# Kernel optimization log

Hardware: AMD Instinct MI355X
Metric: run time of the kernel (lower is better)

## Reference

```python
import jax, jax.numpy as jnp
import numpy as np

HEADS = 4
OUT = 64  # hidden_channels


def gat_conv(x, src, dst, N, W, att_src, att_dst, bias):
    # x: [N, Fin] -> h: [N, H, C]
    h = (x @ W).reshape(N, HEADS, OUT)
    a_s = (h * att_src).sum(-1)  # [N, H]
    a_d = (h * att_dst).sum(-1)  # [N, H]
    logits = jax.nn.leaky_relu(a_s[src] + a_d[dst], negative_slope=0.2)  # [E, H]
    # segment softmax over incoming edges of each destination node
    m = jax.ops.segment_max(logits, dst, num_segments=N)
    e = jnp.exp(logits - m[dst])
    z = jax.ops.segment_sum(e, dst, num_segments=N)
    alpha = e / (z[dst] + 1e-16)
    out = jax.ops.segment_sum(h[src] * alpha[:, :, None], dst, num_segments=N)
    return out.reshape(N, HEADS * OUT) + bias


def setup_inputs() -> dict:
    key = jax.random.key(0)
    ks = jax.random.split(key, 16)
    N, E, F = 50000, 800000, 128
    HC = HEADS * OUT  # 256
    s = 0.1
    return {
        "x": jax.random.normal(ks[0], (N, F), jnp.float32),
        "edge_index": jax.random.randint(ks[1], (2, E), 0, N, dtype=jnp.int32),
        "W1": jax.random.normal(ks[2], (F, HC), jnp.float32) * s,
        "as1": jax.random.normal(ks[3], (1, HEADS, OUT), jnp.float32) * s,
        "ad1": jax.random.normal(ks[4], (1, HEADS, OUT), jnp.float32) * s,
        "b1": jnp.zeros((HC,), jnp.float32),
        "W2": jax.random.normal(ks[5], (HC, HC), jnp.float32) * s,
        "as2": jax.random.normal(ks[6], (1, HEADS, OUT), jnp.float32) * s,
        "ad2": jax.random.normal(ks[7], (1, HEADS, OUT), jnp.float32) * s,
        "b2": jnp.zeros((HC,), jnp.float32),
        "lw1": jax.random.normal(ks[8], (HC, OUT), jnp.float32) * s,
        "lb1": jnp.zeros((OUT,), jnp.float32),
        "lw2": jax.random.normal(ks[9], (OUT, 2), jnp.float32) * s,
        "lb2": jnp.zeros((2,), jnp.float32),
    }


def reference(x, edge_index, W1, as1, ad1, b1, W2, as2, ad2, b2, lw1, lb1, lw2, lb2):
    N = x.shape[0]
    # PyG GATConv default add_self_loops=True
    loop = jnp.arange(N, dtype=edge_index.dtype)
    src = jnp.concatenate([edge_index[0], loop])
    dst = jnp.concatenate([edge_index[1], loop])
    h = jax.nn.elu(gat_conv(x, src, dst, N, W1, as1, ad1, b1))
    # dropout is identity at inference
    h = jax.nn.elu(gat_conv(h, src, dst, N, W2, as2, ad2, b2))
    h = jax.nn.relu(h @ lw1 + lb1)
    return jax.nn.log_softmax(h @ lw2 + lb2, axis=1)
```

## Files before the change

kernel.cpp:

```cpp
#include <hip/hip_runtime.h>
#include <math.h>


typedef __attribute__((ext_vector_type(8))) _Float16 half8v;
typedef __attribute__((ext_vector_type(4))) float f32x4;

__device__ __forceinline__ float lrelu(float x) { return x > 0.f ? x : 0.2f * x; }
__device__ __forceinline__ float elu1(float x) { return x > 0.f ? x : (__expf(x) - 1.f); }

__global__ void convert_weights_kernel(const float* __restrict__ W1, const float* __restrict__ W2,
                                       const float* __restrict__ lw1,
                                       _Float16* __restrict__ o1, _Float16* __restrict__ o2,
                                       _Float16* __restrict__ o3, int* __restrict__ indeg,
                                       int N) {
  int t = blockIdx.x * blockDim.x + threadIdx.x;
  if (t < 32768) {
    int n = t >> 7, k = t & 127;
    o1[t] = (_Float16)W1[(long)k * 256 + n];
  } else if (t < 98304) {
    int i = t - 32768;
    int n = i >> 8, k = i & 255;
    o2[i] = (_Float16)W2[(long)k * 256 + n];
  } else if (t < 114688) {
    int i = t - 98304;
    int n = i >> 8, k = i & 255;
    o3[i] = (_Float16)lw1[(long)k * 64 + n];
  } else if (t < 114688 + N) {
    indeg[t - 114688] = 0;
  }
}

__global__ void count_kernel(const int* __restrict__ dst, int E, int* __restrict__ indeg) {
  int e = blockIdx.x * blockDim.x + threadIdx.x;
  if (e < E) atomicAdd(&indeg[dst[e]], 1);
}

__global__ void scan_block_kernel(const int* __restrict__ in, int* __restrict__ incl,
                                  int* __restrict__ bsum, int N) {
  __shared__ int wsum[16];
  int gid = blockIdx.x * 1024 + threadIdx.x;
  int lane = threadIdx.x & 63, w = threadIdx.x >> 6;
  int v = (gid < N) ? in[gid] : 0;
  int sv = v;
#pragma unroll
  for (int o = 1; o < 64; o <<= 1) {
    int t = __shfl_up(sv, o);
    if (lane >= o) sv += t;
  }
  if (lane == 63) wsum[w] = sv;
  __syncthreads();
  if (w == 0) {
    int bs = (lane < 16) ? wsum[lane] : 0;
#pragma unroll
    for (int o = 1; o < 16; o <<= 1) {
      int t = __shfl_up(bs, o);
      if (lane >= o) bs += t;
    }
    if (lane < 16) wsum[lane] = bs;
  }
  __syncthreads();
  if (w > 0) sv += wsum[w - 1];
  if (gid < N) incl[gid] = sv;
  if (threadIdx.x == 1023) bsum[blockIdx.x] = sv;
}

__global__ void scan_finalize_kernel(const int* __restrict__ in, const int* __restrict__ incl,
                                     const int* __restrict__ bsum, int* __restrict__ off,
                                     int* __restrict__ cursor, int N) {
  int gid = blockIdx.x * blockDim.x + threadIdx.x;
  if (gid >= N) return;
  int b = gid >> 10;
  int carry = 0;
  for (int k = 0; k < b; ++k) carry += bsum[k];
  int ic = incl[gid] + carry;
  off[gid + 1] = ic;
  cursor[gid] = ic - in[gid];
  if (gid == 0) off[0] = 0;
}

__global__ void fill_kernel(const int* __restrict__ src, const int* __restrict__ dst, int E,
                            int* __restrict__ cursor, int* __restrict__ csr_src) {
  int e = blockIdx.x * blockDim.x + threadIdx.x;
  if (e < E) {
    int pos = atomicAdd(&cursor[dst[e]], 1);
    csr_src[pos] = src[e];
  }
}

template <typename AT>
__launch_bounds__(256)
__global__ void mfma_gemm_attn_kernel(const AT* __restrict__ A,
                                      const _Float16* __restrict__ B,
                                      const float* __restrict__ att_s,
                                      const float* __restrict__ att_d,
                                      _Float16* __restrict__ C,
                                      float* __restrict__ a_s, float* __restrict__ a_d,
                                      int M, int K) {
  __shared__ _Float16 As[128][40];
  __shared__ _Float16 Bs[128][40];
  int tid = threadIdx.x;
  int bm = blockIdx.y * 128, bn = blockIdx.x * 128;
  int lane = tid & 63, wave = tid >> 6;
  int srow = tid >> 2, sch = (tid & 3) * 8;
  const AT* Ap0 = A + (long)(bm + srow) * K + sch;
  const AT* Ap1 = A + (long)(bm + 64 + srow) * K + sch;
  const _Float16* Bp0 = B + (long)(bn + srow) * K + sch;
  const _Float16* Bp1 = B + (long)(bn + 64 + srow) * K + sch;
  bool aok0 = (bm + srow) < M, aok1 = (bm + 64 + srow) < M;
  int fm = lane & 15, fq = lane >> 4;
  int wr = wave >> 1, wc = wave & 1;
  f32x4 acc[4][4];
#pragma unroll
  for (int mi = 0; mi < 4; ++mi)
#pragma unroll
    for (int ni = 0; ni < 4; ++ni) acc[mi][ni] = (f32x4){0.f, 0.f, 0.f, 0.f};
  for (int k0 = 0; k0 < K; k0 += 32) {
    half8v a80 = {0, 0, 0, 0, 0, 0, 0, 0}, a81 = {0, 0, 0, 0, 0, 0, 0, 0};
    if constexpr (sizeof(AT) == 4) {
      if (aok0) {
        float4 f0 = *(const float4*)(Ap0 + k0);
        float4 f1 = *(const float4*)(Ap0 + k0 + 4);
        a80 = (half8v){(_Float16)f0.x, (_Float16)f0.y, (_Float16)f0.z, (_Float16)f0.w,
                       (_Float16)f1.x, (_Float16)f1.y, (_Float16)f1.z, (_Float16)f1.w};
      }
      if (aok1) {
        float4 f0 = *(const float4*)(Ap1 + k0);
        float4 f1 = *(const float4*)(Ap1 + k0 + 4);
        a81 = (half8v){(_Float16)f0.x, (_Float16)f0.y, (_Float16)f0.z, (_Float16)f0.w,
                       (_Float16)f1.x, (_Float16)f1.y, (_Float16)f1.z, (_Float16)f1.w};
      }
    } else {
      if (aok0) a80 = *(const half8v*)(Ap0 + k0);
      if (aok1) a81 = *(const half8v*)(Ap1 + k0);
    }
    uint4 vb0 = *(const uint4*)(Bp0 + k0);
    uint4 vb1 = *(const uint4*)(Bp1 + k0);
    *(half8v*)&As[srow][sch] = a80;
    *(half8v*)&As[64 + srow][sch] = a81;
    *(uint4*)&Bs[srow][sch] = vb0;
    *(uint4*)&Bs[64 + srow][sch] = vb1;
    __syncthreads();
    half8v ah[4], bh[4];
#pragma unroll
    for (int i = 0; i < 4; ++i) ah[i] = *(const half8v*)&As[wr * 64 + i * 16 + fm][fq * 8];
#pragma unroll
    for (int i = 0; i < 4; ++i) bh[i] = *(const half8v*)&Bs[wc * 64 + i * 16 + fm][fq * 8];
#pragma unroll
    for (int mi = 0; mi < 4; ++mi)
#pragma unroll
      for (int ni = 0; ni < 4; ++ni)
        acc[mi][ni] = __builtin_amdgcn_mfma_f32_16x16x32_f16(ah[mi], bh[ni], acc[mi][ni], 0, 0, 0);
    __syncthreads();
  }
  int headi = blockIdx.x * 2 + wc;
  int cbase = bn + wc * 64;
  float asv[4], adv[4];
#pragma unroll
  for (int ni = 0; ni < 4; ++ni) {
    int col = cbase + ni * 16 + fm;
    asv[ni] = att_s[col];
    adv[ni] = att_d[col];
  }
#pragma unroll
  for (int mi = 0; mi < 4; ++mi) {
    int rowb = bm + wr * 64 + mi * 16 + fq * 4;
#pragma unroll
    for (int r = 0; r < 4; ++r) {
      int row = rowb + r;
      float sp = 0.f, dp = 0.f;
#pragma unroll
      for (int ni = 0; ni < 4; ++ni) {
        float v = acc[mi][ni][r];
        sp = fmaf(v, asv[ni], sp);
        dp = fmaf(v, adv[ni], dp);
        if (row < M) C[(long)row * 256 + cbase + ni * 16 + fm] = (_Float16)v;
      }
#pragma unroll
      for (int o = 1; o < 16; o <<= 1) {
        sp += __shfl_xor(sp, o);
        dp += __shfl_xor(dp, o);
      }
      if (fm == 0 && row < M) {
        a_s[(long)row * 4 + headi] = sp;
        a_d[(long)row * 4 + headi] = dp;
      }
    }
  }
}

__launch_bounds__(256)
__global__ void head_mfma_kernel(const _Float16* __restrict__ A, const _Float16* __restrict__ B,
                                 const float* __restrict__ lb1, const float* __restrict__ lw2,
                                 const float* __restrict__ lb2, float* __restrict__ out, int M) {
  __shared__ _Float16 As[128][40];
  __shared__ _Float16 Bs[64][40];
  int tid = threadIdx.x;
  int bm = blockIdx.x * 128;
  int lane = tid & 63, wave = tid >> 6;
  int srow = tid >> 2, sch = (tid & 3) * 8;
  const _Float16* Ap0 = A + (long)(bm + srow) * 256 + sch;
  const _Float16* Ap1 = A + (long)(bm + 64 + srow) * 256 + sch;
  const _Float16* Bp = B + (long)srow * 256 + sch;
  bool aok0 = (bm + srow) < M, aok1 = (bm + 64 + srow) < M;
  int fm = lane & 15, fq = lane >> 4;
  f32x4 acc[2][4];
#pragma unroll
  for (int mi = 0; mi < 2; ++mi)
#pragma unroll
    for (int ni = 0; ni < 4; ++ni) acc[mi][ni] = (f32x4){0.f, 0.f, 0.f, 0.f};
  for (int k0 = 0; k0 < 256; k0 += 32) {
    half8v a80 = {0, 0, 0, 0, 0, 0, 0, 0}, a81 = {0, 0, 0, 0, 0, 0, 0, 0};
    if (aok0) a80 = *(const half8v*)(Ap0 + k0);
    if (aok1) a81 = *(const half8v*)(Ap1 + k0);
    uint4 vb = *(const uint4*)(Bp + k0);
    *(half8v*)&As[srow][sch] = a80;
    *(half8v*)&As[64 + srow][sch] = a81;
    *(uint4*)&Bs[srow][sch] = vb;
    __syncthreads();
    half8v ah[2], bh[4];
#pragma unroll
    for (int mi = 0; mi < 2; ++mi)
      ah[mi] = *(const half8v*)&As[wave * 32 + mi * 16 + fm][fq * 8];
#pragma unroll
    for (int ni = 0; ni < 4; ++ni) bh[ni] = *(const half8v*)&Bs[ni * 16 + fm][fq * 8];
#pragma unroll
    for (int mi = 0; mi < 2; ++mi)
#pragma unroll
      for (int ni = 0; ni < 4; ++ni)
        acc[mi][ni] = __builtin_amdgcn_mfma_f32_16x16x32_f16(ah[mi], bh[ni], acc[mi][ni], 0, 0, 0);
    __syncthreads();
  }
  float lb1c[4], w20[4], w21[4];
#pragma unroll
  for (int ni = 0; ni < 4; ++ni) {
    int col = ni * 16 + fm;
    lb1c[ni] = lb1[col];
    w20[ni] = lw2[col * 2 + 0];
    w21[ni] = lw2[col * 2 + 1];
  }
  float b20 = lb2[0], b21 = lb2[1];
#pragma unroll
  for (int mi = 0; mi < 2; ++mi) {
#pragma unroll
    for (int r = 0; r < 4; ++r) {
      float v0 = 0.f, v1 = 0.f;
#pragma unroll
      for (int ni = 0; ni < 4; ++ni) {
        float s = fmaxf(acc[mi][ni][r] + lb1c[ni], 0.f);
        v0 = fmaf(s, w20[ni], v0);
        v1 = fmaf(s, w21[ni], v1);
      }
#pragma unroll
      for (int o = 1; o < 16; o <<= 1) {
        v0 += __shfl_xor(v0, o);
        v1 += __shfl_xor(v1, o);
      }
      if (fm == 0) {
        int row = bm + wave * 32 + mi * 16 + fq * 4 + r;
        if (row < M) {
          v0 += b20;
          v1 += b21;
          float mx = fmaxf(v0, v1);
          float ls = mx + logf(expf(v0 - mx) + expf(v1 - mx));
          out[(long)row * 2 + 0] = v0 - ls;
          out[(long)row * 2 + 1] = v1 - ls;
        }
      }
    }
  }
}

__launch_bounds__(256)
__global__ void gat_aggregate_exp_kernel(const _Float16* __restrict__ h,
                                         const float* __restrict__ a_s,
                                         const float* __restrict__ a_d,
                                         const int* __restrict__ off,
                                         const int* __restrict__ csr_src,
                                         const float* __restrict__ bias,
                                         _Float16* __restrict__ outp, int N) {
  int wid = (blockIdx.x * blockDim.x + threadIdx.x) >> 6;
  int lane = threadIdx.x & 63;
  if (wid >= N) return;
  int c = lane & 31, hlf = lane >> 5, head4 = c >> 3;
  int h1 = lane & 3, sl1 = lane >> 2;
  int beg = off[wid], cnt = off[wid + 1] - beg;
  float ad_h1 = a_d[wid * 4 + h1];
  float psl = __expf(lrelu(a_s[wid * 4 + h1] + ad_h1));
  float pself = __shfl(psl, head4);
  float z = 0.f;
  float acc[8] = {};
  if (hlf == 0) {
    z = pself;
    half8v sr = *(const half8v*)(h + (long)wid * 256 + c * 8);
#pragma unroll
    for (int i = 0; i < 8; ++i) acc[i] = pself * (float)sr[i];
  }
  for (int c0 = 0; c0 < cnt; c0 += 16) {
    int i2 = c0 + (lane & 15);
    int sv = (i2 < cnt) ? csr_src[beg + i2] : 0;
    int i1 = c0 + sl1;
    int spi = __shfl(sv, sl1);
    float pv = (i1 < cnt) ? __expf(lrelu(a_s[(long)spi * 4 + h1] + ad_h1)) : 0.f;
#pragma unroll 4
    for (int j = 0; j < 16; j += 2) {
      if (c0 + j >= cnt) break;
      int e = j + hlf;
      int s = __shfl(sv, e);
      float p = __shfl(pv, e * 4 + head4);
      z += p;
      half8v rv = *(const half8v*)(h + (long)s * 256 + c * 8);
      acc[0] = fmaf(p, (float)rv[0], acc[0]);
      acc[1] = fmaf(p, (float)rv[1], acc[1]);
      acc[2] = fmaf(p, (float)rv[2], acc[2]);
      acc[3] = fmaf(p, (float)rv[3], acc[3]);
      acc[4] = fmaf(p, (float)rv[4], acc[4]);
      acc[5] = fmaf(p, (float)rv[5], acc[5]);
      acc[6] = fmaf(p, (float)rv[6], acc[6]);
      acc[7] = fmaf(p, (float)rv[7], acc[7]);
    }
  }
  z += __shfl_xor(z, 32);
#pragma unroll
  for (int i = 0; i < 8; ++i) acc[i] += __shfl_xor(acc[i], 32);
  if (hlf == 0) {
    float inv = 1.f / z;
    half8v o;
#pragma unroll
    for (int i = 0; i < 8; ++i) o[i] = (_Float16)elu1(fmaf(acc[i], inv, bias[c * 8 + i]));
    *(half8v*)(outp + (long)wid * 256 + c * 8) = o;
  }
}

static inline int cdiv(int a, int b) { return (a + b - 1) / b; }

extern "C" void kernel_launch(void* const* d_in, const int* in_sizes, int n_in,
                              void* d_out, int out_size, void* d_ws, size_t ws_size,
                              hipStream_t stream) {
  const float* x = (const float*)d_in[0];
  const int* ei = (const int*)d_in[1];
  const float* W1 = (const float*)d_in[2];
  const float* as1 = (const float*)d_in[3];
  const float* ad1 = (const float*)d_in[4];
  const float* b1 = (const float*)d_in[5];
  const float* W2 = (const float*)d_in[6];
  const float* as2 = (const float*)d_in[7];
  const float* ad2 = (const float*)d_in[8];
  const float* b2 = (const float*)d_in[9];
  const float* lw1 = (const float*)d_in[10];
  const float* lb1 = (const float*)d_in[11];
  const float* lw2 = (const float*)d_in[12];
  const float* lb2 = (const float*)d_in[13];
  float* out = (float*)d_out;

  int N = in_sizes[0] / 128;
  int E = in_sizes[1] / 2;
  int Mp = cdiv(N, 128) * 128;

  char* ws = (char*)d_ws;
  _Float16* Wt1 = (_Float16*)ws; ws += 256 * 128 * 2;
  _Float16* Wt2 = (_Float16*)ws; ws += 256 * 256 * 2;
  _Float16* WL = (_Float16*)ws; ws += 64 * 256 * 2;
  _Float16* C = (_Float16*)ws; ws += (size_t)Mp * 256 * 2;
  _Float16* h2 = (_Float16*)ws; ws += (size_t)Mp * 256 * 2;
  float* aS = (float*)ws; ws += (size_t)N * 4 * 4;
  float* aD = (float*)ws; ws += (size_t)N * 4 * 4;
  int* csr_src = (int*)ws; ws += (size_t)E * 4;
  int* indeg = (int*)ws; ws += (size_t)N * 4;
  int* cursor = (int*)ws; ws += (size_t)N * 4;
  int* off = (int*)ws; ws += (size_t)(N + 4) * 4;
  int* incl = (int*)ws; ws += (size_t)N * 4;
  int* bsum = (int*)ws; ws += 64 * 4;

  const int* e_src = ei;
  const int* e_dst = ei + E;
  int nb = cdiv(N, 1024);

  convert_weights_kernel<<<cdiv(114688 + N, 256), 256, 0, stream>>>(W1, W2, lw1, Wt1, Wt2, WL,
                                                                    indeg, N);

  count_kernel<<<cdiv(E, 256), 256, 0, stream>>>(e_dst, E, indeg);
  scan_block_kernel<<<nb, 1024, 0, stream>>>(indeg, incl, bsum, N);
  scan_finalize_kernel<<<cdiv(N, 256), 256, 0, stream>>>(indeg, incl, bsum, off, cursor, N);
  fill_kernel<<<cdiv(E, 256), 256, 0, stream>>>(e_src, e_dst, E, cursor, csr_src);

  mfma_gemm_attn_kernel<float><<<dim3(2, Mp / 128), 256, 0, stream>>>(x, Wt1, as1, ad1, C, aS, aD,
                                                                      N, 128);
  gat_aggregate_exp_kernel<<<cdiv(N, 4), 256, 0, stream>>>(C, aS, aD, off, csr_src, b1, h2, N);

  mfma_gemm_attn_kernel<_Float16><<<dim3(2, Mp / 128), 256, 0, stream>>>(h2, Wt2, as2, ad2, C, aS,
                                                                         aD, N, 256);
  gat_aggregate_exp_kernel<<<cdiv(N, 4), 256, 0, stream>>>(C, aS, aD, off, csr_src, b2, h2, N);

  head_mfma_kernel<<<Mp / 128, 256, 0, stream>>>(h2, WL, lb1, lw2, lb2, out, N);
}
```

Baseline: 380.1 us.

## Preload whole B panel into LDS and stream A fragments directly from global

The GEMM+attention and head kernels now load the full K-depth slice of the weight panel (64 columns) into shared memory once. Each wave then reads its A fragments straight from global memory into MFMA registers, with no per-k-step A staging and no barriers inside the k loop. The GEMM grid changes from 128x128 tiles to 128-row x 64-column tiles (one head per block). This removes per-iteration syncthreads and LDS traffic for A. In exchange, A rows are reread by four column-panel blocks, and the uncoalesced per-lane row loads may cost more memory traffic.

```diff
diff --git a/kernel.cpp b/kernel.cpp
--- a/kernel.cpp
+++ b/kernel.cpp
@@ -87,73 +87,71 @@
   }
 }
 
-template <typename AT>
+template <typename AT, int K>
 __launch_bounds__(256)
-__global__ void mfma_gemm_attn_kernel(const AT* __restrict__ A,
-                                      const _Float16* __restrict__ B,
-                                      const float* __restrict__ att_s,
-                                      const float* __restrict__ att_d,
-                                      _Float16* __restrict__ C,
-                                      float* __restrict__ a_s, float* __restrict__ a_d,
-                                      int M, int K) {
-  __shared__ _Float16 As[128][40];
-  __shared__ _Float16 Bs[128][40];
+__global__ void gemm_stream_attn_kernel(const AT* __restrict__ A,
+                                        const _Float16* __restrict__ B,
+                                        const float* __restrict__ att_s,
+                                        const float* __restrict__ att_d,
+                                        _Float16* __restrict__ C,
+                                        float* __restrict__ a_s, float* __restrict__ a_d,
+                                        int M) {
+  constexpr int NK = K / 32;
+  __shared__ _Float16 Bs[NK][64][40];
   int tid = threadIdx.x;
-  int bm = blockIdx.y * 128, bn = blockIdx.x * 128;
   int lane = tid & 63, wave = tid >> 6;
-  int srow = tid >> 2, sch = (tid & 3) * 8;
-  const AT* Ap0 = A + (long)(bm + srow) * K + sch;
-  const AT* Ap1 = A + (long)(bm + 64 + srow) * K + sch;
-  const _Float16* Bp0 = B + (long)(bn + srow) * K + sch;
-  const _Float16* Bp1 = B + (long)(bn + 64 + srow) * K + sch;
-  bool aok0 = (bm + srow) < M, aok1 = (bm + 64 + srow) < M;
+  int bm = blockIdx.y * 128;
+  int panel = blockIdx.x;
+  int cbase = panel * 64;
+  {
+    int col = tid >> 2, kc = (tid & 3) * 8;
+    const _Float16* Bp = B + (long)(cbase + col) * K + kc;
+#pragma unroll
+    for (int ks = 0; ks < NK; ++ks)
+      *(uint4*)&Bs[ks][col][kc] = *(const uint4*)(Bp + ks * 32);
+  }
+  __syncthreads();
   int fm = lane & 15, fq = lane >> 4;
-  int wr = wave >> 1, wc = wave & 1;
-  f32x4 acc[4][4];
-#pragma unroll
-  for (int mi = 0; mi < 4; ++mi)
+  int row0 = bm + wave * 32 + fm;
+  int row1 = row0 + 16;
+  const AT* Ap0 = A + (long)row0 * K + fq * 8;
+  const AT* Ap1 = A + (long)row1 * K + fq * 8;
+  bool ok0 = row0 < M, ok1 = row1 < M;
+  f32x4 acc[2][4];
+#pragma unroll
+  for (int mi = 0; mi < 2; ++mi)
 #pragma unroll
     for (int ni = 0; ni < 4; ++ni) acc[mi][ni] = (f32x4){0.f, 0.f, 0.f, 0.f};
-  for (int k0 = 0; k0 < K; k0 += 32) {
-    half8v a80 = {0, 0, 0, 0, 0, 0, 0, 0}, a81 = {0, 0, 0, 0, 0, 0, 0, 0};
+#pragma unroll
+  for (int ks = 0; ks < NK; ++ks) {
+    half8v a0 = {0, 0, 0, 0, 0, 0, 0, 0}, a1 = {0, 0, 0, 0, 0, 0, 0, 0};
     if constexpr (sizeof(AT) == 4) {
-      if (aok0) {
-        float4 f0 = *(const float4*)(Ap0 + k0);
-        float4 f1 = *(const float4*)(Ap0 + k0 + 4);
-        a80 = (half8v){(_Float16)f0.x, (_Float16)f0.y, (_Float16)f0.z, (_Float16)f0.w,
-                       (_Float16)f1.x, (_Float16)f1.y, (_Float16)f1.z, (_Float16)f1.w};
-      }
-      if (aok1) {
-        float4 f0 = *(const float4*)(Ap1 + k0);
-        float4 f1 = *(const float4*)(Ap1 + k0 + 4);
-        a81 = (half8v){(_Float16)f0.x, (_Float16)f0.y, (_Float16)f0.z, (_Float16)f0.w,
-                       (_Float16)f1.x, (_Float16)f1.y, (_Float16)f1.z, (_Float16)f1.w};
+      if (ok0) {
+        float4 f0 = *(const float4*)(Ap0 + ks * 32);
+        float4 f1 = *(const float4*)(Ap0 + ks * 32 + 4);
+        a0 = (half8v){(_Float16)f0.x, (_Float16)f0.y, (_Float16)f0.z, (_Float16)f0.w,
+                      (_Float16)f1.x, (_Float16)f1.y, (_Float16)f1.z, (_Float16)f1.w};
+      }
+      if (ok1) {
+        float4 f0 = *(const float4*)(Ap1 + ks * 32);
+        float4 f1 = *(const float4*)(Ap1 + ks * 32 + 4);
+        a1 = (half8v){(_Float16)f0.x, (_Float16)f0.y, (_Float16)f0.z, (_Float16)f0.w,
+                      (_Float16)f1.x, (_Float16)f1.y, (_Float16)f1.z, (_Float16)f1.w};
       }
     } else {
-      if (aok0) a80 = *(const half8v*)(Ap0 + k0);
-      if (aok1) a81 = *(const half8v*)(Ap1 + k0);
-    }
-    uint4 vb0 = *(const uint4*)(Bp0 + k0);
-    uint4 vb1 = *(const uint4*)(Bp1 + k0);
-    *(half8v*)&As[srow][sch] = a80;
-    *(half8v*)&As[64 + srow][sch] = a81;
-    *(uint4*)&Bs[srow][sch] = vb0;
-    *(uint4*)&Bs[64 + srow][sch] = vb1;
-    __syncthreads();
-    half8v ah[4], bh[4];
-#pragma unroll
-    for (int i = 0; i < 4; ++i) ah[i] = *(const half8v*)&As[wr * 64 + i * 16 + fm][fq * 8];
-#pragma unroll
-    for (int i = 0; i < 4; ++i) bh[i] = *(const half8v*)&Bs[wc * 64 + i * 16 + fm][fq * 8];
-#pragma unroll
-    for (int mi = 0; mi < 4; ++mi)
-#pragma unroll
-      for (int ni = 0; ni < 4; ++ni)
-        acc[mi][ni] = __builtin_amdgcn_mfma_f32_16x16x32_f16(ah[mi], bh[ni], acc[mi][ni], 0, 0, 0);
-    __syncthreads();
-  }
-  int headi = blockIdx.x * 2 + wc;
-  int cbase = bn + wc * 64;
+      if (ok0) a0 = *(const half8v*)(Ap0 + ks * 32);
+      if (ok1) a1 = *(const half8v*)(Ap1 + ks * 32);
+    }
+    half8v bh[4];
+#pragma unroll
+    for (int ni = 0; ni < 4; ++ni) bh[ni] = *(const half8v*)&Bs[ks][ni * 16 + fm][fq * 8];
+#pragma unroll
+    for (int ni = 0; ni < 4; ++ni) {
+      acc[0][ni] = __builtin_amdgcn_mfma_f32_16x16x32_f16(a0, bh[ni], acc[0][ni], 0, 0, 0);
+      acc[1][ni] = __builtin_amdgcn_mfma_f32_16x16x32_f16(a1, bh[ni], acc[1][ni], 0, 0, 0);
+    }
+  }
+  int headi = panel;
   float asv[4], adv[4];
 #pragma unroll
   for (int ni = 0; ni < 4; ++ni) {
@@ -162,8 +160,8 @@
     adv[ni] = att_d[col];
   }
 #pragma unroll
-  for (int mi = 0; mi < 4; ++mi) {
-    int rowb = bm + wr * 64 + mi * 16 + fq * 4;
+  for (int mi = 0; mi < 2; ++mi) {
+    int rowb = bm + wave * 32 + mi * 16 + fq * 4;
 #pragma unroll
     for (int r = 0; r < 4; ++r) {
       int row = rowb + r;
@@ -189,46 +187,46 @@
 }
 
 __launch_bounds__(256)
-__global__ void head_mfma_kernel(const _Float16* __restrict__ A, const _Float16* __restrict__ B,
-                                 const float* __restrict__ lb1, const float* __restrict__ lw2,
-                                 const float* __restrict__ lb2, float* __restrict__ out, int M) {
-  __shared__ _Float16 As[128][40];
-  __shared__ _Float16 Bs[64][40];
+__global__ void head_stream_kernel(const _Float16* __restrict__ A, const _Float16* __restrict__ B,
+                                   const float* __restrict__ lb1, const float* __restrict__ lw2,
+                                   const float* __restrict__ lb2, float* __restrict__ out, int M) {
+  constexpr int NK = 8;
+  __shared__ _Float16 Bs[NK][64][40];
   int tid = threadIdx.x;
+  int lane = tid & 63, wave = tid >> 6;
   int bm = blockIdx.x * 128;
-  int lane = tid & 63, wave = tid >> 6;
-  int srow = tid >> 2, sch = (tid & 3) * 8;
-  const _Float16* Ap0 = A + (long)(bm + srow) * 256 + sch;
-  const _Float16* Ap1 = A + (long)(bm + 64 + srow) * 256 + sch;
-  const _Float16* Bp = B + (long)srow * 256 + sch;
-  bool aok0 = (bm + srow) < M, aok1 = (bm + 64 + srow) < M;
+  {
+    int col = tid >> 2, kc = (tid & 3) * 8;
+    const _Float16* Bp = B + (long)col * 256 + kc;
+#pragma unroll
+    for (int ks = 0; ks < NK; ++ks)
+      *(uint4*)&Bs[ks][col][kc] = *(const uint4*)(Bp + ks * 32);
+  }
+  __syncthreads();
   int fm = lane & 15, fq = lane >> 4;
+  int row0 = bm + wave * 32 + fm;
+  int row1 = row0 + 16;
+  const _Float16* Ap0 = A + (long)row0 * 256 + fq * 8;
+  const _Float16* Ap1 = A + (long)row1 * 256 + fq * 8;
+  bool ok0 = row0 < M, ok1 = row1 < M;
   f32x4 acc[2][4];
 #pragma unroll
   for (int mi = 0; mi < 2; ++mi)
 #pragma unroll
     for (int ni = 0; ni < 4; ++ni) acc[mi][ni] = (f32x4){0.f, 0.f, 0.f, 0.f};
-  for (int k0 = 0; k0 < 256; k0 += 32) {
-    half8v a80 = {0, 0, 0, 0, 0, 0, 0, 0}, a81 = {0, 0, 0, 0, 0, 0, 0, 0};
-    if (aok0) a80 = *(const half8v*)(Ap0 + k0);
-    if (aok1) a81 = *(const half8v*)(Ap1 + k0);
-    uint4 vb = *(const uint4*)(Bp + k0);
-    *(half8v*)&As[srow][sch] = a80;
-    *(half8v*)&As[64 + srow][sch] = a81;
-    *(uint4*)&Bs[srow][sch] = vb;
-    __syncthreads();
-    half8v ah[2], bh[4];
-#pragma unroll
-    for (int mi = 0; mi < 2; ++mi)
-      ah[mi] = *(const half8v*)&As[wave * 32 + mi * 16 + fm][fq * 8];
-#pragma unroll
-    for (int ni = 0; ni < 4; ++ni) bh[ni] = *(const half8v*)&Bs[ni * 16 + fm][fq * 8];
-#pragma unroll
-    for (int mi = 0; mi < 2; ++mi)
-#pragma unroll
-      for (int ni = 0; ni < 4; ++ni)
-        acc[mi][ni] = __builtin_amdgcn_mfma_f32_16x16x32_f16(ah[mi], bh[ni], acc[mi][ni], 0, 0, 0);
-    __syncthreads();
+#pragma unroll
+  for (int ks = 0; ks < NK; ++ks) {
+    half8v a0 = {0, 0, 0, 0, 0, 0, 0, 0}, a1 = {0, 0, 0, 0, 0, 0, 0, 0};
+    if (ok0) a0 = *(const half8v*)(Ap0 + ks * 32);
+    if (ok1) a1 = *(const half8v*)(Ap1 + ks * 32);
+    half8v bh[4];
+#pragma unroll
+    for (int ni = 0; ni < 4; ++ni) bh[ni] = *(const half8v*)&Bs[ks][ni * 16 + fm][fq * 8];
+#pragma unroll
+    for (int ni = 0; ni < 4; ++ni) {
+      acc[0][ni] = __builtin_amdgcn_mfma_f32_16x16x32_f16(a0, bh[ni], acc[0][ni], 0, 0, 0);
+      acc[1][ni] = __builtin_amdgcn_mfma_f32_16x16x32_f16(a1, bh[ni], acc[1][ni], 0, 0, 0);
+    }
   }
   float lb1c[4], w20[4], w21[4];
 #pragma unroll
@@ -383,13 +381,13 @@
   scan_finalize_kernel<<<cdiv(N, 256), 256, 0, stream>>>(indeg, incl, bsum, off, cursor, N);
   fill_kernel<<<cdiv(E, 256), 256, 0, stream>>>(e_src, e_dst, E, cursor, csr_src);
 
-  mfma_gemm_attn_kernel<float><<<dim3(2, Mp / 128), 256, 0, stream>>>(x, Wt1, as1, ad1, C, aS, aD,
-                                                                      N, 128);
+  gemm_stream_attn_kernel<float, 128><<<dim3(4, Mp / 128), 256, 0, stream>>>(x, Wt1, as1, ad1, C,
+                                                                             aS, aD, N);
   gat_aggregate_exp_kernel<<<cdiv(N, 4), 256, 0, stream>>>(C, aS, aD, off, csr_src, b1, h2, N);
 
-  mfma_gemm_attn_kernel<_Float16><<<dim3(2, Mp / 128), 256, 0, stream>>>(h2, Wt2, as2, ad2, C, aS,
-                                                                         aD, N, 256);
+  gemm_stream_attn_kernel<_Float16, 256><<<dim3(4, Mp / 128), 256, 0, stream>>>(h2, Wt2, as2, ad2,
+                                                                                C, aS, aD, N);
   gat_aggregate_exp_kernel<<<cdiv(N, 4), 256, 0, stream>>>(C, aS, aD, off, csr_src, b2, h2, N);
 
-  head_mfma_kernel<<<Mp / 128, 256, 0, stream>>>(h2, WL, lb1, lw2, lb2, out, N);
-}
+  head_stream_kernel<<<Mp / 128, 256, 0, stream>>>(h2, WL, lb1, lw2, lb2, out, N);
+}
```

Result: no change. 382.8 us (+0.7%).
